# Optimization experiments

Hardware: AMD Instinct MI355X
Metric: run time of the kernel (lower is better)

## Reference

```python
import jax, jax.numpy as jnp
import numpy as np
import math

N_EMBD = 768
N_HEAD = 12
B, T, S = 8, 1024, 257
HEAD_DIM = N_EMBD // N_HEAD


def _ln(x, g, b, eps=1e-5):
    m = jnp.mean(x, axis=-1, keepdims=True)
    v = jnp.mean(jnp.square(x - m), axis=-1, keepdims=True)
    return (x - m) * jax.lax.rsqrt(v + eps) * g + b


def _heads(t, n_head):
    b, s, c = t.shape
    return t.reshape(b, s, n_head, c // n_head).transpose(0, 2, 1, 3)  # (B,H,S,D)


def setup_inputs() -> dict:
    key = jax.random.key(0)
    ks = jax.random.split(key, 12)
    sc = 0.02
    d, h4 = N_EMBD, 4 * N_EMBD
    return {
        "x": jax.random.normal(ks[0], (B, T, d), jnp.float32),
        "encoder_x": jax.random.normal(ks[1], (B, S, d), jnp.float32),
        "ln1_g": jnp.ones((d,), jnp.float32), "ln1_b": jnp.zeros((d,), jnp.float32),
        "ln2_g": jnp.ones((d,), jnp.float32), "ln2_b": jnp.zeros((d,), jnp.float32),
        "ln3_g": jnp.ones((d,), jnp.float32), "ln3_b": jnp.zeros((d,), jnp.float32),
        "attn_w": jax.random.normal(ks[2], (d, 3 * d), jnp.float32) * sc,
        "attn_b": jnp.zeros((3 * d,), jnp.float32),
        "attn_proj_w": jax.random.normal(ks[3], (d, d), jnp.float32) * sc,
        "attn_proj_b": jnp.zeros((d,), jnp.float32),
        "cross_w": jax.random.normal(ks[4], (d, 3 * d), jnp.float32) * sc,
        "cross_b": jnp.zeros((3 * d,), jnp.float32),
        "cross_proj_w": jax.random.normal(ks[5], (d, d), jnp.float32) * sc,
        "cross_proj_b": jnp.zeros((d,), jnp.float32),
        "fc_w": jax.random.normal(ks[6], (d, h4), jnp.float32) * sc,
        "fc_b": jnp.zeros((h4,), jnp.float32),
        "proj_w": jax.random.normal(ks[7], (h4, d), jnp.float32) * sc,
        "proj_b": jnp.zeros((d,), jnp.float32),
    }


def reference(x, encoder_x, ln1_g, ln1_b, ln2_g, ln2_b, ln3_g, ln3_b,
              attn_w, attn_b, attn_proj_w, attn_proj_b,
              cross_w, cross_b, cross_proj_w, cross_proj_b,
              fc_w, fc_b, proj_w, proj_b):
    d = N_EMBD
    scale = 1.0 / math.sqrt(HEAD_DIM)

    # --- causal self-attention ---
    h = _ln(x, ln1_g, ln1_b)
    qkv = h @ attn_w + attn_b
    q, k, v = (_heads(t, N_HEAD) for t in jnp.split(qkv, 3, axis=-1))
    att = jnp.einsum('bhqd,bhkd->bhqk', q, k) * scale
    t = x.shape[1]
    causal = jnp.tril(jnp.ones((t, t), bool))
    att = jnp.where(causal[None, None], att, -jnp.inf)
    att = jax.nn.softmax(att, axis=-1)
    o = jnp.einsum('bhqk,bhkd->bhqd', att, v)
    o = o.transpose(0, 2, 1, 3).reshape(x.shape)
    x = x + o @ attn_proj_w + attn_proj_b

    # --- cross-attention (shared c_attn for q from x, k/v from encoder) ---
    h = _ln(x, ln2_g, ln2_b)
    q = _heads((h @ cross_w + cross_b)[..., :d], N_HEAD)
    ekv = encoder_x @ cross_w + cross_b
    k = _heads(ekv[..., d:2 * d], N_HEAD)
    v = _heads(ekv[..., 2 * d:], N_HEAD)
    att = jax.nn.softmax(jnp.einsum('bhqd,bhkd->bhqk', q, k) * scale, axis=-1)
    o = jnp.einsum('bhqk,bhkd->bhqd', att, v)
    o = o.transpose(0, 2, 1, 3).reshape(x.shape)
    x = x + o @ cross_proj_w + cross_proj_b

    # --- MLP (GELU tanh) ---
    h = _ln(x, ln3_g, ln3_b)
    h = jax.nn.gelu(h @ fc_w + fc_b, approximate=True)
    x = x + h @ proj_w + proj_b
    return x
```

## Files before the change

### kernel.cpp

```cpp
#include <hip/hip_runtime.h>

typedef __bf16 bf16x8 __attribute__((ext_vector_type(8)));
typedef float  f32x4  __attribute__((ext_vector_type(4)));
typedef unsigned short u16;

#define N_EMBD 768
#define T_LEN 1024
#define S_LEN 257
#define S_PAD 320
#define BATCH 8
#define NH 12
#define BH (BATCH*NH)
#define HD 64

__device__ __forceinline__ u16 f2b(float f){
  union{ __bf16 h; u16 u; } v; v.h=(__bf16)f; return v.u;
}
__device__ __forceinline__ float b2f(u16 h){
  union{unsigned u; float f;} v; v.u=((unsigned)h)<<16;
  return v.f;
}
__device__ __forceinline__ void gl_lds16(const void* g, void* l){
  __builtin_amdgcn_global_load_lds((const __attribute__((address_space(1))) void*)g,
                                   (__attribute__((address_space(3))) void*)l, 16, 0, 0);
}

template<int C> __device__ __forceinline__ float dpp_mov_f(float x){
  union{float f;int i;} u; u.f=x;
  u.i = __builtin_amdgcn_mov_dpp(u.i, C, 0xf, 0xf, true);
  return u.f;
}
__device__ __forceinline__ float red16_add(float x){
  x = x + dpp_mov_f<0xB1>(x);
  x = x + dpp_mov_f<0x4E>(x);
  x = x + dpp_mov_f<0x141>(x);
  x = x + dpp_mov_f<0x140>(x);
  return x;
}

__global__ void prep_all(const float* __restrict__ s0,const float* __restrict__ s1,
                         const float* __restrict__ s2,const float* __restrict__ s3,
                         const float* __restrict__ s4,const float* __restrict__ s5,
                         u16* __restrict__ d0,u16* __restrict__ d1,
                         u16* __restrict__ d2,u16* __restrict__ d3,
                         u16* __restrict__ d4,u16* __restrict__ d5,
                         const float* __restrict__ enc, u16* __restrict__ enc_bf,
                         const float* __restrict__ xin, const float* __restrict__ g1,
                         const float* __restrict__ b1, u16* __restrict__ hbuf,
                         const float* __restrict__ attn_b, const float* __restrict__ cross_b,
                         float* __restrict__ sb_attn, float* __restrict__ sb_cross){
  __shared__ u16 tile[64][68];
  int id=blockIdx.x;
  if(id>=5894){
    int i=(id-5894)*256+threadIdx.x;
    if(i<2304)      sb_attn[i]       = attn_b[i]       *((i     <768)?0.125f:1.f);
    else if(i<4608) sb_cross[i-2304] = cross_b[i-2304] *((i-2304<768)?0.125f:1.f);
    return;
  }
  if(id>=3846){
    int row  = (id-3846)*4 + (threadIdx.x>>6);
    int lane = threadIdx.x&63;
    size_t base = (size_t)row*N_EMBD;
    float v[12];
#pragma unroll
    for(int p=0;p<3;p++){
      int col = p*256 + lane*4;
      float4 f = *(const float4*)&xin[base+col];
      v[p*4]=f.x; v[p*4+1]=f.y; v[p*4+2]=f.z; v[p*4+3]=f.w;
    }
    float s=0.f, s2=0.f;
#pragma unroll
    for(int i=0;i<12;i++){ s+=v[i]; s2+=v[i]*v[i]; }
#pragma unroll
    for(int off=1; off<64; off<<=1){ s += __shfl_xor(s,off); s2 += __shfl_xor(s2,off); }
    float mean = s*(1.f/N_EMBD);
    float var  = s2*(1.f/N_EMBD) - mean*mean;
    float rstd = rsqrtf(var + 1e-5f);
#pragma unroll
    for(int p=0;p<3;p++){
      int col = p*256 + lane*4;
#pragma unroll
      for(int j=0;j<4;j++){
        hbuf[base+col+j] = f2b((v[p*4+j]-mean)*rstd*g1[col+j] + b1[col+j]);
      }
    }
    return;
  }
  if(id>=2304){
    int i = (id-2304)*256 + threadIdx.x;
    float4 f = *(const float4*)&enc[i*4];
    ushort4 u; u.x=f2b(f.x); u.y=f2b(f.y); u.z=f2b(f.z); u.w=f2b(f.w);
    *(ushort4*)&enc_bf[i*4] = u;
    return;
  }
  const float* in; u16* out; int K,N,t;
  if(id<432)      {in=s0;out=d0;K=768;N=2304;t=id;}
  else if(id<864) {in=s1;out=d1;K=768;N=2304;t=id-432;}
  else if(id<1008){in=s2;out=d2;K=768;N=768;t=id-864;}
  else if(id<1152){in=s3;out=d3;K=768;N=768;t=id-1008;}
  else if(id<1728){in=s4;out=d4;K=768;N=3072;t=id-1152;}
  else            {in=s5;out=d5;K=3072;N=768;t=id-1728;}
  int tiles_n=N>>6;
  int k0=(t/tiles_n)<<6, n0=(t%tiles_n)<<6;
  float qs = (id<864 && n0<768) ? 0.125f : 1.f;
  int tr = threadIdx.x>>4;
  int tc = (threadIdx.x&15)*4;
#pragma unroll
  for(int i=0;i<4;i++){
    float4 f = *(const float4*)&in[(size_t)(k0+tr+i*16)*N + n0 + tc];
    tile[tr+i*16][tc+0]=f2b(f.x*qs); tile[tr+i*16][tc+1]=f2b(f.y*qs);
    tile[tr+i*16][tc+2]=f2b(f.z*qs); tile[tr+i*16][tc+3]=f2b(f.w*qs);
  }
  __syncthreads();
#pragma unroll
  for(int i=0;i<4;i++){
    int n = n0+tr+i*16;
    ushort4 u;
    u.x=tile[tc+0][tr+i*16]; u.y=tile[tc+1][tr+i*16];
    u.z=tile[tc+2][tr+i*16]; u.w=tile[tc+3][tr+i*16];
    *(ushort4*)&out[(size_t)n*K + k0 + tc] = u;
  }
}

__global__ void ln_kernel(const float* __restrict__ x, const float* __restrict__ g,
                          const float* __restrict__ bta, u16* __restrict__ out){
  int row  = blockIdx.x*4 + (threadIdx.x>>6);
  int lane = threadIdx.x&63;
  size_t base = (size_t)row*N_EMBD;
  float v[12];
#pragma unroll
  for(int p=0;p<3;p++){
    int col = p*256 + lane*4;
    float4 f = *(const float4*)&x[base+col];
    v[p*4]=f.x; v[p*4+1]=f.y; v[p*4+2]=f.z; v[p*4+3]=f.w;
  }
  float s=0.f, s2=0.f;
#pragma unroll
  for(int i=0;i<12;i++){ s+=v[i]; s2+=v[i]*v[i]; }
#pragma unroll
  for(int off=1; off<64; off<<=1){ s += __shfl_xor(s,off); s2 += __shfl_xor(s2,off); }
  float mean = s*(1.f/N_EMBD);
  float var  = s2*(1.f/N_EMBD) - mean*mean;
  float rstd = rsqrtf(var + 1e-5f);
#pragma unroll
  for(int p=0;p<3;p++){
    int col = p*256 + lane*4;
#pragma unroll
    for(int j=0;j<4;j++){
      out[base+col+j] = f2b((v[p*4+j]-mean)*rstd*g[col+j] + bta[col+j]);
    }
  }
}

enum { M_QKV_SELF=0, M_Q_CROSS=1, M_KV_CROSS=2, M_RESID_F32=3,
       M_RESID_INPLACE=4, M_GELU=5, M_RESID_OUT=6 };

template<int MODE, int BN>
__device__ __forceinline__ void gemm_body(u16* __restrict__ As, u16* __restrict__ Bs,
                        const u16* __restrict__ A, const u16* __restrict__ Wt,
                        const float* __restrict__ bias,
                        void* out0, void* out1, void* out2, const void* resid,
                        int M, int K, int Ntiles, int Mtl, int bid){
  constexpr int MI = (BN==128)?4:2;
  int tid=threadIdx.x, wave=tid>>6, lane=tid&63;

  int mt, nt;
  if((Mtl&7)==0){
    int xcd=bid&7, j=bid>>3, bpx=Mtl>>3;
    int band=j/Ntiles; nt=j-band*Ntiles; mt=xcd*bpx+band;
  } else { mt=bid/Ntiles; nt=bid-mt*Ntiles; }
  int m0=mt*128, n0=nt*BN;

  int wm = (BN==128)? (wave>>1)*64 : wave*32;
  int wn = (BN==128)? (wave&1)*64  : 0;
  int lrow=lane&15, quad=lane>>4;
  f32x4 acc[MI][4];
  f32x4 z = {0.f,0.f,0.f,0.f};
#pragma unroll
  for(int i=0;i<MI;i++)
#pragma unroll
    for(int j=0;j<4;j++) acc[i][j]=z;

  int srow  = wave*8 + (lane>>3);
  int c_src = (lane&7) ^ ((lane>>3)&7);
  int pa = quad ^ (lrow&7);

  const u16* ap[4];
#pragma unroll
  for(int i=0;i<4;i++){
    int ga = min(m0 + i*32 + srow, M-1);
    ap[i] = A + (size_t)ga*K + c_src*8;
  }
  const u16* bp[BN/32];
#pragma unroll
  for(int i=0;i<BN/32;i++)
    bp[i] = Wt + (size_t)(n0 + i*32 + srow)*K + c_src*8;

  for(int k0=0;k0<K;k0+=64){
#pragma unroll
    for(int i=0;i<4;i++)
      gl_lds16(ap[i] + k0, &As[(i*32+wave*8)*64]);
#pragma unroll
    for(int i=0;i<BN/32;i++)
      gl_lds16(bp[i] + k0, &Bs[(i*32+wave*8)*64]);
    __syncthreads();
    bf16x8 af[MI][2], bfr[4][2];
#pragma unroll
    for(int i=0;i<MI;i++){
      const u16* ab=&As[(wm+i*16+lrow)*64];
      af[i][0]=*(const bf16x8*)(ab+pa*8);
      af[i][1]=*(const bf16x8*)(ab+(pa^4)*8);
    }
#pragma unroll
    for(int i=0;i<4;i++){
      const u16* bb=&Bs[(wn+i*16+lrow)*64];
      bfr[i][0]=*(const bf16x8*)(bb+pa*8);
      bfr[i][1]=*(const bf16x8*)(bb+(pa^4)*8);
    }
#pragma unroll
    for(int h=0;h<2;h++)
#pragma unroll
      for(int mi=0;mi<MI;mi++)
#pragma unroll
        for(int ni=0;ni<4;ni++)
          acc[mi][ni] = __builtin_amdgcn_mfma_f32_16x16x32_bf16(af[mi][h], bfr[ni][h], acc[mi][ni], 0,0,0);
    __syncthreads();
  }

#pragma unroll
  for(int ni=0;ni<4;ni++){
    int n = n0 + wn + ni*16 + lrow;
    float bv = bias[n];
#pragma unroll
    for(int mi=0;mi<MI;mi++){
      int mbase = m0 + wm + mi*16 + quad*4;
      float cr[4];
#pragma unroll
      for(int r=0;r<4;r++) cr[r]=acc[mi][ni][r]+bv;

      if constexpr (MODE==M_QKV_SELF){
        int part=n/768, nn=n-part*768;
        int hh=nn>>6, dd=nn&63;
        int b=mbase>>10, t0=mbase&1023;
        size_t bh=(size_t)(b*NH+hh);
        if(part==0){
#pragma unroll
          for(int r=0;r<4;r++) ((u16*)out0)[(bh*T_LEN+t0+r)*HD+dd]=f2b(cr[r]);
        } else if(part==1){
#pragma unroll
          for(int r=0;r<4;r++) ((u16*)out1)[(bh*T_LEN+t0+r)*HD+dd]=f2b(cr[r]);
        } else {
          ushort4 pk; pk.x=f2b(cr[0]); pk.y=f2b(cr[1]); pk.z=f2b(cr[2]); pk.w=f2b(cr[3]);
          *(ushort4*)&((u16*)out2)[(bh*HD+dd)*T_LEN+t0]=pk;
        }
      } else if constexpr (MODE==M_Q_CROSS){
        int b=mbase>>10, t0=mbase&1023;
        int hh=n>>6, dd=n&63;
        size_t bh=(size_t)(b*NH+hh);
#pragma unroll
        for(int r=0;r<4;r++) ((u16*)out0)[(bh*T_LEN+t0+r)*HD+dd]=f2b(cr[r]);
      } else if constexpr (MODE==M_KV_CROSS){
        int part=n/768, nn=n-part*768;
        int hh=nn>>6, dd=nn&63;
#pragma unroll
        for(int r=0;r<4;r++){
          int m=mbase+r;
          if(m<M){
            int b=m/S_LEN, s=m-b*S_LEN;
            size_t bh=(size_t)(b*NH+hh);
            if(part==0) ((u16*)out0)[(bh*S_PAD+s)*HD+dd]=f2b(cr[r]);
            else        ((u16*)out1)[(bh*HD+dd)*S_PAD+s]=f2b(cr[r]);
          }
        }
      } else if constexpr (MODE==M_RESID_F32){
        const float* x=(const float*)resid;
#pragma unroll
        for(int r=0;r<4;r++){ int m=mbase+r;
          ((float*)out0)[(size_t)m*768+n]=x[(size_t)m*768+n]+cr[r]; }
      } else if constexpr (MODE==M_RESID_INPLACE){
#pragma unroll
        for(int r=0;r<4;r++){ int m=mbase+r;
          ((float*)out0)[(size_t)m*768+n]+=cr[r]; }
      } else if constexpr (MODE==M_GELU){
#pragma unroll
        for(int r=0;r<4;r++){
          int m=mbase+r;
          float uu=cr[r];
          float zz=0.7978845608028654f*(uu+0.044715f*uu*uu*uu);
          float e=__expf(fminf(2.f*zz, 80.f));
          ((u16*)out0)[(size_t)m*3072+n]=f2b(uu*e*__builtin_amdgcn_rcpf(e+1.f));
        }
      } else {
        const float* x=(const float*)resid;
#pragma unroll
        for(int r=0;r<4;r++){ int m=mbase+r;
          ((float*)out0)[(size_t)m*768+n]=x[(size_t)m*768+n]+cr[r]; }
      }
    }
  }
}

template<int MODE, int BN>
__global__ __launch_bounds__(256,3)
void gemm_bt(const u16* __restrict__ A, const u16* __restrict__ Wt,
             const float* __restrict__ bias,
             void* out0, void* out1, void* out2, const void* resid,
             int M, int K, int Ntiles){
  __shared__ u16 As[128*64];
  __shared__ u16 Bs[BN*64];
  gemm_body<MODE,BN>(As,Bs,A,Wt,bias,out0,out1,out2,resid,M,K,Ntiles,
                     gridDim.x/Ntiles, blockIdx.x);
}

__global__ __launch_bounds__(256,3)
void gemm_cross(const u16* __restrict__ hbuf, const u16* __restrict__ cwT,
                const float* __restrict__ sbc, const u16* __restrict__ encbf,
                void* Qc, void* Kc, void* Vct){
  __shared__ u16 As[128*64];
  __shared__ u16 Bs[64*64];
  if(blockIdx.x<768)
    gemm_body<M_Q_CROSS,64>(As,Bs,hbuf,cwT,sbc,Qc,nullptr,nullptr,nullptr,
                            8192,768,12, 64, blockIdx.x);
  else
    gemm_body<M_KV_CROSS,64>(As,Bs,encbf,cwT+768*768,sbc+768,Kc,Vct,nullptr,nullptr,
                             2056,768,24, 17, blockIdx.x-768);
}

template<bool CAUSAL>
__global__ __launch_bounds__(256,2)
void flash_attn(const u16* __restrict__ Q, const u16* __restrict__ Kk,
                const u16* __restrict__ V, u16* __restrict__ O,
                int Skey, int Spad){
  __shared__ u16 KT[2][64*64];
  __shared__ u16 VT[2][64*64];
  __shared__ u16 Plds[4][16][72];
  int bh = blockIdx.x % BH;
  int qbi= blockIdx.x / BH;
  int qb = CAUSAL ? (15-qbi) : qbi;
  int b=bh/NH, hh=bh-b*NH;
  int wave=threadIdx.x>>6, lane=threadIdx.x&63;
  int lrow=lane&15, quad=lane>>4;
  const u16* Qp=Q+(size_t)bh*T_LEN*HD;
  const u16* Kp=Kk+(size_t)bh*Spad*HD;
  const u16* Vp=V+(size_t)bh*HD*Spad;
  u16* Op=O+(size_t)b*T_LEN*N_EMBD+hh*HD;
  int q0 = qb*64 + wave*16;

  int r0    = wave*8 + (lane>>3);
  int c_src = (lane&7) ^ ((lane>>3)&7);

  bf16x8 aq0=*(const bf16x8*)&Qp[(size_t)(q0+lrow)*HD + quad*8];
  bf16x8 aq1=*(const bf16x8*)&Qp[(size_t)(q0+lrow)*HD + 32 + quad*8];

  f32x4 oacc[4];
  f32x4 z={0.f,0.f,0.f,0.f};
#pragma unroll
  for(int i=0;i<4;i++) oacc[i]=z;
  float lsum[4]={0.f,0.f,0.f,0.f};

  int nt = CAUSAL ? (qb+1) : ((Skey+63)>>6);

  {
    gl_lds16(Kp + (size_t)r0*HD        + c_src*8, &KT[0][(wave*8)*64]);
    gl_lds16(Kp + (size_t)(r0+32)*HD   + c_src*8, &KT[0][(32+wave*8)*64]);
    gl_lds16(Vp + (size_t)r0*Spad      + c_src*8, &VT[0][(wave*8)*64]);
    gl_lds16(Vp + (size_t)(r0+32)*Spad + c_src*8, &VT[0][(32+wave*8)*64]);
  }
  __syncthreads();

  int p0 = quad ^ (lrow&7);

  for(int it=0; it<nt; it++){
    int bb = it&1;
    int kt = it*64;
    if(it+1<nt){
      int ktn=(it+1)*64;
      gl_lds16(Kp + (size_t)(ktn+r0)*HD      + c_src*8, &KT[bb^1][(wave*8)*64]);
      gl_lds16(Kp + (size_t)(ktn+r0+32)*HD   + c_src*8, &KT[bb^1][(32+wave*8)*64]);
      gl_lds16(Vp + (size_t)r0*Spad      + ktn + c_src*8, &VT[bb^1][(wave*8)*64]);
      gl_lds16(Vp + (size_t)(r0+32)*Spad + ktn + c_src*8, &VT[bb^1][(32+wave*8)*64]);
    }
    f32x4 s[4];
#pragma unroll
    for(int g=0;g<4;g++){
      const u16* kb=&KT[bb][(g*16+lrow)*64];
      bf16x8 bk0=*(const bf16x8*)(kb+p0*8);
      bf16x8 bk1=*(const bf16x8*)(kb+(p0^4)*8);
      s[g]=z;
      s[g]=__builtin_amdgcn_mfma_f32_16x16x32_bf16(aq0,bk0,s[g],0,0,0);
      s[g]=__builtin_amdgcn_mfma_f32_16x16x32_bf16(aq1,bk1,s[g],0,0,0);
    }
    bool domask = (it==nt-1);
#pragma unroll
    for(int r=0;r<4;r++){
      float sv0=s[0][r], sv1=s[1][r], sv2=s[2][r], sv3=s[3][r];
      if(domask){
        if(CAUSAL){
          int q=q0+quad*4+r;
          if(kt+lrow    >q) sv0=-3.0e38f;
          if(kt+16+lrow >q) sv1=-3.0e38f;
          if(kt+32+lrow >q) sv2=-3.0e38f;
          if(kt+48+lrow >q) sv3=-3.0e38f;
        } else {
          if(kt+lrow    >=Skey) sv0=-3.0e38f;
          if(kt+16+lrow >=Skey) sv1=-3.0e38f;
          if(kt+32+lrow >=Skey) sv2=-3.0e38f;
          if(kt+48+lrow >=Skey) sv3=-3.0e38f;
        }
      }
      float p0e=__expf(sv0), p1e=__expf(sv1);
      float p2e=__expf(sv2), p3e=__expf(sv3);
      lsum[r] += (p0e+p1e)+(p2e+p3e);
      Plds[wave][quad*4+r][lrow]    = f2b(p0e);
      Plds[wave][quad*4+r][16+lrow] = f2b(p1e);
      Plds[wave][quad*4+r][32+lrow] = f2b(p2e);
      Plds[wave][quad*4+r][48+lrow] = f2b(p3e);
    }
    bf16x8 ap0=*(const bf16x8*)&Plds[wave][lrow][quad*8];
    bf16x8 ap1=*(const bf16x8*)&Plds[wave][lrow][32+quad*8];
#pragma unroll
    for(int dt=0;dt<4;dt++){
      const u16* vb=&VT[bb][(dt*16+lrow)*64];
      bf16x8 bv0=*(const bf16x8*)(vb+p0*8);
      bf16x8 bv1=*(const bf16x8*)(vb+(p0^4)*8);
      oacc[dt]=__builtin_amdgcn_mfma_f32_16x16x32_bf16(ap0,bv0,oacc[dt],0,0,0);
      oacc[dt]=__builtin_amdgcn_mfma_f32_16x16x32_bf16(ap1,bv1,oacc[dt],0,0,0);
    }
    __syncthreads();
  }
  float linv[4];
#pragma unroll
  for(int r=0;r<4;r++) linv[r]=1.f/red16_add(lsum[r]);
#pragma unroll
  for(int dt=0;dt<4;dt++){
#pragma unroll
    for(int r=0;r<4;r++){
      int q=q0+quad*4+r;
      Op[(size_t)q*N_EMBD + dt*16 + lrow]=f2b(oacc[dt][r]*linv[r]);
    }
  }
}

extern "C" void kernel_launch(void* const* d_in, const int* in_sizes, int n_in,
                              void* d_out, int out_size, void* d_ws, size_t ws_size,
                              hipStream_t stream){
  const float* x_in   =(const float*)d_in[0];
  const float* enc    =(const float*)d_in[1];
  const float* ln1_g  =(const float*)d_in[2];
  const float* ln1_b  =(const float*)d_in[3];
  const float* ln2_g  =(const float*)d_in[4];
  const float* ln2_b  =(const float*)d_in[5];
  const float* ln3_g  =(const float*)d_in[6];
  const float* ln3_b  =(const float*)d_in[7];
  const float* attn_w =(const float*)d_in[8];
  const float* attn_b =(const float*)d_in[9];
  const float* attn_pw=(const float*)d_in[10];
  const float* attn_pb=(const float*)d_in[11];
  const float* cross_w=(const float*)d_in[12];
  const float* cross_b=(const float*)d_in[13];
  const float* cross_pw=(const float*)d_in[14];
  const float* cross_pb=(const float*)d_in[15];
  const float* fc_w   =(const float*)d_in[16];
  const float* fc_b   =(const float*)d_in[17];
  const float* proj_w =(const float*)d_in[18];
  const float* proj_b =(const float*)d_in[19];

  char* ws=(char*)d_ws;
  u16*  attn_wT  =(u16*)(ws + 0);
  u16*  cross_wT =(u16*)(ws + 3538944);
  u16*  attn_pwT =(u16*)(ws + 7077888);
  u16*  cross_pwT=(u16*)(ws + 8257536);
  u16*  fc_wT    =(u16*)(ws + 9437184);
  u16*  proj_wT  =(u16*)(ws + 14155776);
  float* xcur    =(float*)(ws + 18874368);
  u16*  hbuf     =(u16*)(ws + 44040192);
  u16*  Qs       =(u16*)(ws + 56623104);
  u16*  Ks       =(u16*)(ws + 69206016);
  u16*  Vst      =(u16*)(ws + 81788928);
  u16*  Qc       =(u16*)(ws + 94371840);
  u16*  hf       =(u16*)(ws + 56623104);
  u16*  Kc       =(u16*)(ws + 106954752);
  u16*  Vct      =(u16*)(ws + 110886912);
  u16*  enc_bf   =(u16*)(ws + 114819072);
  float* sb_attn =(float*)(ws + 117977088);
  float* sb_cross=(float*)(ws + 117986304);

  dim3 blk(256);
  prep_all<<<5912,blk,0,stream>>>(attn_w, cross_w, attn_pw, cross_pw, fc_w, proj_w,
                                  attn_wT, cross_wT, attn_pwT, cross_pwT, fc_wT, proj_wT,
                                  enc, enc_bf, x_in, ln1_g, ln1_b, hbuf,
                                  attn_b, cross_b, sb_attn, sb_cross);

  gemm_bt<M_QKV_SELF,128><<<1152,blk,0,stream>>>(hbuf, attn_wT, sb_attn,
      Qs, Ks, Vst, nullptr, 8192, 768, 18);
  flash_attn<true><<<1536,blk,0,stream>>>(Qs, Ks, Vst, hbuf, 1024, 1024);
  gemm_bt<M_RESID_F32,64><<<768,blk,0,stream>>>(hbuf, attn_pwT, attn_pb,
      xcur, nullptr, nullptr, x_in, 8192, 768, 12);

  ln_kernel<<<2048,blk,0,stream>>>(xcur, ln2_g, ln2_b, hbuf);
  gemm_cross<<<1176,blk,0,stream>>>(hbuf, cross_wT, sb_cross, enc_bf, Qc, Kc, Vct);
  flash_attn<false><<<1536,blk,0,stream>>>(Qc, Kc, Vct, hbuf, S_LEN, S_PAD);
  gemm_bt<M_RESID_INPLACE,64><<<768,blk,0,stream>>>(hbuf, cross_pwT, cross_pb,
      xcur, nullptr, nullptr, nullptr, 8192, 768, 12);

  ln_kernel<<<2048,blk,0,stream>>>(xcur, ln3_g, ln3_b, hbuf);
  gemm_bt<M_GELU,128><<<1536,blk,0,stream>>>(hbuf, fc_wT, fc_b,
      hf, nullptr, nullptr, nullptr, 8192, 768, 24);
  gemm_bt<M_RESID_OUT,64><<<768,blk,0,stream>>>(hf, proj_wT, proj_b,
      d_out, nullptr, nullptr, xcur, 8192, 3072, 12);
}
```

Baseline: 424.9 us.

## Load K/V fragments directly from global memory in flash attention, drop LDS staging

The flash attention kernel stops staging K and V tiles in double-buffered shared memory and instead loads each wave's MFMA operand fragments straight from global memory. This removes the per-iteration block barrier and most of the kernel's LDS use, and the occupancy hint is raised from 2 to 4 blocks per CU. In exchange, each of the four waves now fetches the same K/V data separately through the cache, with no prefetch of the next tile to hide load latency.

```diff
diff --git a/kernel.cpp b/kernel.cpp
--- a/kernel.cpp
+++ b/kernel.cpp
@@ -327,12 +327,10 @@
 }
 
 template<bool CAUSAL>
-__global__ __launch_bounds__(256,2)
+__global__ __launch_bounds__(256,4)
 void flash_attn(const u16* __restrict__ Q, const u16* __restrict__ Kk,
                 const u16* __restrict__ V, u16* __restrict__ O,
                 int Skey, int Spad){
-  __shared__ u16 KT[2][64*64];
-  __shared__ u16 VT[2][64*64];
   __shared__ u16 Plds[4][16][72];
   int bh = blockIdx.x % BH;
   int qbi= blockIdx.x / BH;
@@ -346,9 +344,6 @@
   u16* Op=O+(size_t)b*T_LEN*N_EMBD+hh*HD;
   int q0 = qb*64 + wave*16;
 
-  int r0    = wave*8 + (lane>>3);
-  int c_src = (lane&7) ^ ((lane>>3)&7);
-
   bf16x8 aq0=*(const bf16x8*)&Qp[(size_t)(q0+lrow)*HD + quad*8];
   bf16x8 aq1=*(const bf16x8*)&Qp[(size_t)(q0+lrow)*HD + 32 + quad*8];
 
@@ -360,32 +355,17 @@
 
   int nt = CAUSAL ? (qb+1) : ((Skey+63)>>6);
 
-  {
-    gl_lds16(Kp + (size_t)r0*HD        + c_src*8, &KT[0][(wave*8)*64]);
-    gl_lds16(Kp + (size_t)(r0+32)*HD   + c_src*8, &KT[0][(32+wave*8)*64]);
-    gl_lds16(Vp + (size_t)r0*Spad      + c_src*8, &VT[0][(wave*8)*64]);
-    gl_lds16(Vp + (size_t)(r0+32)*Spad + c_src*8, &VT[0][(32+wave*8)*64]);
-  }
-  __syncthreads();
-
-  int p0 = quad ^ (lrow&7);
+  const u16* kb0 = Kp + (size_t)lrow*HD + quad*8;
+  const u16* vb0 = Vp + (size_t)lrow*Spad + quad*8;
 
   for(int it=0; it<nt; it++){
-    int bb = it&1;
     int kt = it*64;
-    if(it+1<nt){
-      int ktn=(it+1)*64;
-      gl_lds16(Kp + (size_t)(ktn+r0)*HD      + c_src*8, &KT[bb^1][(wave*8)*64]);
-      gl_lds16(Kp + (size_t)(ktn+r0+32)*HD   + c_src*8, &KT[bb^1][(32+wave*8)*64]);
-      gl_lds16(Vp + (size_t)r0*Spad      + ktn + c_src*8, &VT[bb^1][(wave*8)*64]);
-      gl_lds16(Vp + (size_t)(r0+32)*Spad + ktn + c_src*8, &VT[bb^1][(32+wave*8)*64]);
-    }
     f32x4 s[4];
 #pragma unroll
     for(int g=0;g<4;g++){
-      const u16* kb=&KT[bb][(g*16+lrow)*64];
-      bf16x8 bk0=*(const bf16x8*)(kb+p0*8);
-      bf16x8 bk1=*(const bf16x8*)(kb+(p0^4)*8);
+      const u16* kp = kb0 + (size_t)(kt+g*16)*HD;
+      bf16x8 bk0=*(const bf16x8*)(kp);
+      bf16x8 bk1=*(const bf16x8*)(kp+32);
       s[g]=z;
       s[g]=__builtin_amdgcn_mfma_f32_16x16x32_bf16(aq0,bk0,s[g],0,0,0);
       s[g]=__builtin_amdgcn_mfma_f32_16x16x32_bf16(aq1,bk1,s[g],0,0,0);
@@ -420,13 +400,12 @@
     bf16x8 ap1=*(const bf16x8*)&Plds[wave][lrow][32+quad*8];
 #pragma unroll
     for(int dt=0;dt<4;dt++){
-      const u16* vb=&VT[bb][(dt*16+lrow)*64];
-      bf16x8 bv0=*(const bf16x8*)(vb+p0*8);
-      bf16x8 bv1=*(const bf16x8*)(vb+(p0^4)*8);
+      const u16* vp = vb0 + (size_t)(dt*16)*Spad + kt;
+      bf16x8 bv0=*(const bf16x8*)(vp);
+      bf16x8 bv1=*(const bf16x8*)(vp+32);
       oacc[dt]=__builtin_amdgcn_mfma_f32_16x16x32_bf16(ap0,bv0,oacc[dt],0,0,0);
       oacc[dt]=__builtin_amdgcn_mfma_f32_16x16x32_bf16(ap1,bv1,oacc[dt],0,0,0);
     }
-    __syncthreads();
   }
   float linv[4];
 #pragma unroll
```

Result: slower. 525.3 us (+23.6%).

## Double flash-attention query tile to 128 rows per block for K/V reuse

Applied to the files above, without the earlier changes.

Each wave now handles two 16-row query subgroups (32 rows), so a block covers 128 queries and the grid is halved. Each K/V tile loaded into LDS is reused across twice as many queries, halving K/V global traffic and LDS fragment reads per query. Causal masking is now evaluated per subgroup, and launch bounds are raised to 3 blocks per SM. In exchange each wave needs more registers for accumulators and scores, and the causal grid has fewer, larger blocks, which worsens load balance.

```diff
diff --git a/kernel.cpp b/kernel.cpp
--- a/kernel.cpp
+++ b/kernel.cpp
@@ -327,16 +327,16 @@
 }
 
 template<bool CAUSAL>
-__global__ __launch_bounds__(256,2)
+__global__ __launch_bounds__(256,3)
 void flash_attn(const u16* __restrict__ Q, const u16* __restrict__ Kk,
                 const u16* __restrict__ V, u16* __restrict__ O,
                 int Skey, int Spad){
   __shared__ u16 KT[2][64*64];
   __shared__ u16 VT[2][64*64];
-  __shared__ u16 Plds[4][16][72];
+  __shared__ u16 Plds[4][32][72];
   int bh = blockIdx.x % BH;
   int qbi= blockIdx.x / BH;
-  int qb = CAUSAL ? (15-qbi) : qbi;
+  int qb = CAUSAL ? (7-qbi) : qbi;
   int b=bh/NH, hh=bh-b*NH;
   int wave=threadIdx.x>>6, lane=threadIdx.x&63;
   int lrow=lane&15, quad=lane>>4;
@@ -344,21 +344,27 @@
   const u16* Kp=Kk+(size_t)bh*Spad*HD;
   const u16* Vp=V+(size_t)bh*HD*Spad;
   u16* Op=O+(size_t)b*T_LEN*N_EMBD+hh*HD;
-  int q0 = qb*64 + wave*16;
+  int q0 = qb*128 + wave*32;
 
   int r0    = wave*8 + (lane>>3);
   int c_src = (lane&7) ^ ((lane>>3)&7);
 
-  bf16x8 aq0=*(const bf16x8*)&Qp[(size_t)(q0+lrow)*HD + quad*8];
-  bf16x8 aq1=*(const bf16x8*)&Qp[(size_t)(q0+lrow)*HD + 32 + quad*8];
-
-  f32x4 oacc[4];
+  bf16x8 aq[2][2];
+#pragma unroll
+  for(int sg=0;sg<2;sg++){
+    aq[sg][0]=*(const bf16x8*)&Qp[(size_t)(q0+sg*16+lrow)*HD + quad*8];
+    aq[sg][1]=*(const bf16x8*)&Qp[(size_t)(q0+sg*16+lrow)*HD + 32 + quad*8];
+  }
+
+  f32x4 oacc[2][4];
   f32x4 z={0.f,0.f,0.f,0.f};
 #pragma unroll
-  for(int i=0;i<4;i++) oacc[i]=z;
-  float lsum[4]={0.f,0.f,0.f,0.f};
-
-  int nt = CAUSAL ? (qb+1) : ((Skey+63)>>6);
+  for(int sg=0;sg<2;sg++)
+#pragma unroll
+    for(int i=0;i<4;i++) oacc[sg][i]=z;
+  float lsum[2][4]={{0.f,0.f,0.f,0.f},{0.f,0.f,0.f,0.f}};
+
+  int nt = CAUSAL ? (2*qb+2) : ((Skey+63)>>6);
 
   {
     gl_lds16(Kp + (size_t)r0*HD        + c_src*8, &KT[0][(wave*8)*64]);
@@ -380,63 +386,82 @@
       gl_lds16(Vp + (size_t)r0*Spad      + ktn + c_src*8, &VT[bb^1][(wave*8)*64]);
       gl_lds16(Vp + (size_t)(r0+32)*Spad + ktn + c_src*8, &VT[bb^1][(32+wave*8)*64]);
     }
-    f32x4 s[4];
+    bf16x8 bk[4][2];
 #pragma unroll
     for(int g=0;g<4;g++){
       const u16* kb=&KT[bb][(g*16+lrow)*64];
-      bf16x8 bk0=*(const bf16x8*)(kb+p0*8);
-      bf16x8 bk1=*(const bf16x8*)(kb+(p0^4)*8);
-      s[g]=z;
-      s[g]=__builtin_amdgcn_mfma_f32_16x16x32_bf16(aq0,bk0,s[g],0,0,0);
-      s[g]=__builtin_amdgcn_mfma_f32_16x16x32_bf16(aq1,bk1,s[g],0,0,0);
-    }
-    bool domask = (it==nt-1);
-#pragma unroll
-    for(int r=0;r<4;r++){
-      float sv0=s[0][r], sv1=s[1][r], sv2=s[2][r], sv3=s[3][r];
-      if(domask){
-        if(CAUSAL){
-          int q=q0+quad*4+r;
-          if(kt+lrow    >q) sv0=-3.0e38f;
-          if(kt+16+lrow >q) sv1=-3.0e38f;
-          if(kt+32+lrow >q) sv2=-3.0e38f;
-          if(kt+48+lrow >q) sv3=-3.0e38f;
-        } else {
-          if(kt+lrow    >=Skey) sv0=-3.0e38f;
-          if(kt+16+lrow >=Skey) sv1=-3.0e38f;
-          if(kt+32+lrow >=Skey) sv2=-3.0e38f;
-          if(kt+48+lrow >=Skey) sv3=-3.0e38f;
+      bk[g][0]=*(const bf16x8*)(kb+p0*8);
+      bk[g][1]=*(const bf16x8*)(kb+(p0^4)*8);
+    }
+    f32x4 sc[2][4];
+#pragma unroll
+    for(int sg=0;sg<2;sg++)
+#pragma unroll
+      for(int g=0;g<4;g++){
+        sc[sg][g]=z;
+        sc[sg][g]=__builtin_amdgcn_mfma_f32_16x16x32_bf16(aq[sg][0],bk[g][0],sc[sg][g],0,0,0);
+        sc[sg][g]=__builtin_amdgcn_mfma_f32_16x16x32_bf16(aq[sg][1],bk[g][1],sc[sg][g],0,0,0);
+      }
+#pragma unroll
+    for(int sg=0;sg<2;sg++){
+      bool dm = CAUSAL ? (kt+63 > q0+sg*16) : (kt+63 >= Skey);
+#pragma unroll
+      for(int r=0;r<4;r++){
+        float sv0=sc[sg][0][r], sv1=sc[sg][1][r], sv2=sc[sg][2][r], sv3=sc[sg][3][r];
+        if(dm){
+          if(CAUSAL){
+            int q=q0+sg*16+quad*4+r;
+            if(kt+lrow    >q) sv0=-3.0e38f;
+            if(kt+16+lrow >q) sv1=-3.0e38f;
+            if(kt+32+lrow >q) sv2=-3.0e38f;
+            if(kt+48+lrow >q) sv3=-3.0e38f;
+          } else {
+            if(kt+lrow    >=Skey) sv0=-3.0e38f;
+            if(kt+16+lrow >=Skey) sv1=-3.0e38f;
+            if(kt+32+lrow >=Skey) sv2=-3.0e38f;
+            if(kt+48+lrow >=Skey) sv3=-3.0e38f;
+          }
         }
+        float p0e=__expf(sv0), p1e=__expf(sv1);
+        float p2e=__expf(sv2), p3e=__expf(sv3);
+        lsum[sg][r] += (p0e+p1e)+(p2e+p3e);
+        Plds[wave][sg*16+quad*4+r][lrow]    = f2b(p0e);
+        Plds[wave][sg*16+quad*4+r][16+lrow] = f2b(p1e);
+        Plds[wave][sg*16+quad*4+r][32+lrow] = f2b(p2e);
+        Plds[wave][sg*16+quad*4+r][48+lrow] = f2b(p3e);
       }
-      float p0e=__expf(sv0), p1e=__expf(sv1);
-      float p2e=__expf(sv2), p3e=__expf(sv3);
-      lsum[r] += (p0e+p1e)+(p2e+p3e);
-      Plds[wave][quad*4+r][lrow]    = f2b(p0e);
-      Plds[wave][quad*4+r][16+lrow] = f2b(p1e);
-      Plds[wave][quad*4+r][32+lrow] = f2b(p2e);
-      Plds[wave][quad*4+r][48+lrow] = f2b(p3e);
-    }
-    bf16x8 ap0=*(const bf16x8*)&Plds[wave][lrow][quad*8];
-    bf16x8 ap1=*(const bf16x8*)&Plds[wave][lrow][32+quad*8];
+    }
+    bf16x8 ap[2][2];
+#pragma unroll
+    for(int sg=0;sg<2;sg++){
+      ap[sg][0]=*(const bf16x8*)&Plds[wave][sg*16+lrow][quad*8];
+      ap[sg][1]=*(const bf16x8*)&Plds[wave][sg*16+lrow][32+quad*8];
+    }
 #pragma unroll
     for(int dt=0;dt<4;dt++){
       const u16* vb=&VT[bb][(dt*16+lrow)*64];
       bf16x8 bv0=*(const bf16x8*)(vb+p0*8);
       bf16x8 bv1=*(const bf16x8*)(vb+(p0^4)*8);
-      oacc[dt]=__builtin_amdgcn_mfma_f32_16x16x32_bf16(ap0,bv0,oacc[dt],0,0,0);
-      oacc[dt]=__builtin_amdgcn_mfma_f32_16x16x32_bf16(ap1,bv1,oacc[dt],0,0,0);
+#pragma unroll
+      for(int sg=0;sg<2;sg++){
+        oacc[sg][dt]=__builtin_amdgcn_mfma_f32_16x16x32_bf16(ap[sg][0],bv0,oacc[sg][dt],0,0,0);
+        oacc[sg][dt]=__builtin_amdgcn_mfma_f32_16x16x32_bf16(ap[sg][1],bv1,oacc[sg][dt],0,0,0);
+      }
     }
     __syncthreads();
   }
-  float linv[4];
-#pragma unroll
-  for(int r=0;r<4;r++) linv[r]=1.f/red16_add(lsum[r]);
-#pragma unroll
-  for(int dt=0;dt<4;dt++){
-#pragma unroll
-    for(int r=0;r<4;r++){
-      int q=q0+quad*4+r;
-      Op[(size_t)q*N_EMBD + dt*16 + lrow]=f2b(oacc[dt][r]*linv[r]);
+#pragma unroll
+  for(int sg=0;sg<2;sg++){
+    float linv[4];
+#pragma unroll
+    for(int r=0;r<4;r++) linv[r]=1.f/red16_add(lsum[sg][r]);
+#pragma unroll
+    for(int dt=0;dt<4;dt++){
+#pragma unroll
+      for(int r=0;r<4;r++){
+        int q=q0+sg*16+quad*4+r;
+        Op[(size_t)q*N_EMBD + dt*16 + lrow]=f2b(oacc[sg][dt][r]*linv[r]);
+      }
     }
   }
 }
@@ -493,13 +518,13 @@
 
   gemm_bt<M_QKV_SELF,128><<<1152,blk,0,stream>>>(hbuf, attn_wT, sb_attn,
       Qs, Ks, Vst, nullptr, 8192, 768, 18);
-  flash_attn<true><<<1536,blk,0,stream>>>(Qs, Ks, Vst, hbuf, 1024, 1024);
+  flash_attn<true><<<768,blk,0,stream>>>(Qs, Ks, Vst, hbuf, 1024, 1024);
   gemm_bt<M_RESID_F32,64><<<768,blk,0,stream>>>(hbuf, attn_pwT, attn_pb,
       xcur, nullptr, nullptr, x_in, 8192, 768, 12);
 
   ln_kernel<<<2048,blk,0,stream>>>(xcur, ln2_g, ln2_b, hbuf);
   gemm_cross<<<1176,blk,0,stream>>>(hbuf, cross_wT, sb_cross, enc_bf, Qc, Kc, Vct);
-  flash_attn<false><<<1536,blk,0,stream>>>(Qc, Kc, Vct, hbuf, S_LEN, S_PAD);
+  flash_attn<false><<<768,blk,0,stream>>>(Qc, Kc, Vct, hbuf, S_LEN, S_PAD);
   gemm_bt<M_RESID_INPLACE,64><<<768,blk,0,stream>>>(hbuf, cross_pwT, cross_pb,
       xcur, nullptr, nullptr, nullptr, 8192, 768, 12);
 
```

After: 418.9 us, median of 2. No clear change (-1.4%).
